# Kernel optimization log

Hardware: AMD Instinct MI355X
Metric: run time of the kernel (lower is better)

Reference implementation:

```python
import jax, jax.numpy as jnp
import numpy as np

EPS = 1e-12  # matches tf.math.l2_normalize epsilon

def _l2n(x, axis=-1):
    return x * jax.lax.rsqrt(jnp.maximum(jnp.sum(x * x, axis=axis, keepdims=True), EPS))


def setup_inputs() -> dict:
    key = jax.random.key(0)
    ks = jax.random.split(key, 8)
    B, T, D, N, M = 16, 1024, 1024, 2048, 256
    s = 1.0 / np.sqrt(D)
    return {
        "memory": jax.random.normal(ks[0], (N, M), jnp.float32),
        "controller_output": jax.random.normal(ks[1], (B, T, D), jnp.float32),
        "Wk": jax.random.normal(ks[2], (D, M), jnp.float32) * s,
        "bk": jnp.zeros((M,), jnp.float32),
        "We": jax.random.normal(ks[3], (D, M), jnp.float32) * s,
        "be": jnp.zeros((M,), jnp.float32),
        "Wa": jax.random.normal(ks[4], (D, M), jnp.float32) * s,
        "ba": jnp.zeros((M,), jnp.float32),
    }


def reference(memory, controller_output, Wk, bk, We, be, Wa, ba):
    B, T, _ = controller_output.shape
    # key: softmax over memory_size dim  -> [B,T,M]
    key = jax.nn.softmax(controller_output @ Wk + bk, axis=-1)
    # tf.keras.losses.cosine_similarity returns NEGATIVE cosine similarity
    kn = _l2n(key)          # [B,T,M]
    mn = _l2n(memory)       # [N,M]
    sims = -jnp.einsum('btm,nm->btn', kn, mn)          # [B,T,N]
    w = jax.nn.softmax(sims, axis=-1)                  # [B,T,N]
    erase = jax.nn.sigmoid(controller_output @ We + be)  # [B,T,M]
    add = jax.nn.relu(controller_output @ Wa + ba)       # [B,T,M]
    # mean over (B,T) of (1 - w*erase)*memory + w*add, without tiling memory:
    inv_bt = 1.0 / (B * T)
    we = jnp.einsum('btn,btm->nm', w, erase) * inv_bt   # mean of w \otimes erase
    wa = jnp.einsum('btn,btm->nm', w, add) * inv_bt     # mean of w \otimes add
    return memory * (1.0 - we) + wa                      # [N,M]
```

## Files before the change

### kernel.cpp

```cpp
#include <hip/hip_runtime.h>

#define DEV __device__ __forceinline__

using f32x4    = __attribute__((ext_vector_type(4))) float;
using bf16x8   = __attribute__((ext_vector_type(8))) short;
using float4_t = __attribute__((ext_vector_type(4))) float;
using ushort4_t = __attribute__((ext_vector_type(4))) unsigned short;
using ushort8_t = __attribute__((ext_vector_type(8))) unsigned short;

DEV unsigned short f2bf(float f) {
    unsigned int u = __builtin_bit_cast(unsigned int, f);
    u = (u + 0x7fffu + ((u >> 16) & 1u)) >> 16;
    return (unsigned short)u;
}
DEV float bf2f(unsigned short h) {
    unsigned int u = ((unsigned int)h) << 16;
    return __builtin_bit_cast(float, u);
}

DEV void gload_lds16(const void* g, void* l) {
    __builtin_amdgcn_global_load_lds((const __attribute__((address_space(1))) void*)g,
                                     (__attribute__((address_space(3))) void*)l, 16, 0, 0);
}

template<int TR, int TC, int NTH>
DEV void stage_tile(const unsigned short* __restrict__ src, long ld, long r0, long c0,
                    unsigned short* lds, int tid) {
    constexpr int LPR = (TC * 2) / 16;
    constexpr int RPI = 64 / LPR;
    constexpr int NISSUE = TR / RPI;
    constexpr int NW = NTH / 64;
    const int wid = tid >> 6, lane = tid & 63;
#pragma unroll
    for (int ii = 0; ii < NISSUE / NW; ++ii) {
        const int i = ii * NW + wid;
        const long row = r0 + (long)i * RPI + (lane / LPR);
        const unsigned short* g = src + row * ld + c0 + (lane % LPR) * 8;
        gload_lds16(g, lds + i * 512);
    }
}

__global__ void k0_cast_co(const float* __restrict__ in, unsigned short* __restrict__ out, long n4) {
    long i = (long)blockIdx.x * 256 + threadIdx.x;
    if (i >= n4) return;
    float4_t v = ((const float4_t*)in)[i];
    ushort4_t o;
#pragma unroll
    for (int j = 0; j < 4; ++j) o[j] = f2bf(v[j]);
    ((ushort4_t*)out)[i] = o;
}

__global__ void k0_prep_w(const float* __restrict__ Wk, const float* __restrict__ We,
                          const float* __restrict__ Wa, unsigned short* __restrict__ WcatT) {
    long idx = (long)blockIdx.x * 256 + threadIdx.x;
    int j = (int)(idx >> 10), d = (int)(idx & 1023);
    const float* W = (j < 256) ? Wk : (j < 512) ? We : Wa;
    int m = j & 255;
    WcatT[idx] = f2bf(W[(long)d * 256 + m]);
}

__global__ __launch_bounds__(256) void k0_mn(const float* __restrict__ memory,
                                             unsigned short* __restrict__ mn,
                                             float* __restrict__ S, int BT) {
    int gid = blockIdx.x * 256 + threadIdx.x;
    if (gid < BT) S[gid] = 0.f;
    int row = blockIdx.x * 4 + (threadIdx.x >> 6);
    int lane = threadIdx.x & 63;
    float4_t v = ((const float4_t*)(memory + (long)row * 256))[lane];
    float ss = v[0]*v[0] + v[1]*v[1] + v[2]*v[2] + v[3]*v[3];
#pragma unroll
    for (int d = 1; d < 64; d <<= 1) ss += __shfl_xor(ss, d);
    float sc = rsqrtf(fmaxf(ss, 1e-12f));
    ushort4_t o;
#pragma unroll
    for (int j = 0; j < 4; ++j) o[j] = f2bf(v[j] * sc);
    ((ushort4_t*)(mn + (long)row * 256))[lane] = o;
}

template<int BM, int BN, int BK>
__global__ __launch_bounds__(256, 3)
void k1_gemm_bias(const unsigned short* __restrict__ A, const unsigned short* __restrict__ BT,
                  float* __restrict__ C, int M, int N, int K,
                  const float* __restrict__ bk, const float* __restrict__ be,
                  const float* __restrict__ ba) {
    __shared__ __align__(16) unsigned short As[BM * BK];
    __shared__ __align__(16) unsigned short Bs[BN * BK];
    const int tid = threadIdx.x, lane = tid & 63, wid = tid >> 6;
    const long m0 = (long)blockIdx.x * BM, n0 = (long)blockIdx.y * BN;
    const int wr = (wid >> 1) * 64, wc = (wid & 1) * 64;
    f32x4 acc[4][4] = {};
    for (int kt = 0; kt < K; kt += BK) {
        stage_tile<BM, BK, 256>(A, K, m0, kt, As, tid);
        stage_tile<BN, BK, 256>(BT, K, n0, kt, Bs, tid);
        __syncthreads();
#pragma unroll
        for (int kk = 0; kk < BK; kk += 32) {
            const int klo = kk + (lane >> 4) * 8;
            bf16x8 af[4], bfr[4];
#pragma unroll
            for (int i = 0; i < 4; ++i) {
                af[i]  = *(const bf16x8*)&As[(wr + i * 16 + (lane & 15)) * BK + klo];
                bfr[i] = *(const bf16x8*)&Bs[(wc + i * 16 + (lane & 15)) * BK + klo];
            }
#pragma unroll
            for (int i = 0; i < 4; ++i)
#pragma unroll
                for (int j = 0; j < 4; ++j)
                    acc[i][j] = __builtin_amdgcn_mfma_f32_16x16x32_bf16(af[i], bfr[j], acc[i][j], 0, 0, 0);
        }
        __syncthreads();
    }
#pragma unroll
    for (int i = 0; i < 4; ++i) {
        const long rbase = m0 + wr + i * 16 + ((lane >> 4) * 4);
#pragma unroll
        for (int j = 0; j < 4; ++j) {
            const long col = n0 + wc + j * 16 + (lane & 15);
            float bias = (col < 256) ? bk[col] : (col < 512) ? be[col - 256] : ba[col - 512];
#pragma unroll
            for (int r = 0; r < 4; ++r)
                C[(rbase + r) * N + col] = acc[i][j][r] + bias;
        }
    }
}

__global__ __launch_bounds__(256) void k2_epilogue(const float* __restrict__ logits,
                                                   unsigned short* __restrict__ kn,
                                                   unsigned short* __restrict__ er,
                                                   unsigned short* __restrict__ ad) {
    const int row = blockIdx.x * 4 + (threadIdx.x >> 6);
    const int lane = threadIdx.x & 63;
    const float* L = logits + (long)row * 768;
    float4_t xk = ((const float4_t*)L)[lane];
    float4_t xe = ((const float4_t*)(L + 256))[lane];
    float4_t xa = ((const float4_t*)(L + 512))[lane];
    float mx = fmaxf(fmaxf(xk[0], xk[1]), fmaxf(xk[2], xk[3]));
#pragma unroll
    for (int d = 1; d < 64; d <<= 1) mx = fmaxf(mx, __shfl_xor(mx, d));
    float e[4]; float ss = 0.f;
#pragma unroll
    for (int j = 0; j < 4; ++j) { e[j] = __expf(xk[j] - mx); ss += e[j] * e[j]; }
#pragma unroll
    for (int d = 1; d < 64; d <<= 1) ss += __shfl_xor(ss, d);
    float sc = rsqrtf(ss);
    ushort4_t ok, oe, oa;
#pragma unroll
    for (int j = 0; j < 4; ++j) {
        ok[j] = f2bf(e[j] * sc);
        oe[j] = f2bf(1.f / (1.f + __expf(-xe[j])));
        oa[j] = f2bf(fmaxf(xa[j], 0.f));
    }
    ((ushort4_t*)(kn + (long)row * 256))[lane] = ok;
    ((ushort4_t*)(er + (long)row * 256))[lane] = oe;
    ((ushort4_t*)(ad + (long)row * 256))[lane] = oa;
}

template<int BM, int BN, int BK>
__global__ __launch_bounds__(256, 3)
void k3_gemm_sims(const unsigned short* __restrict__ A, const unsigned short* __restrict__ BT,
                  unsigned short* __restrict__ ET, float* __restrict__ S,
                  int M, int N, int K) {
    __shared__ __align__(16) unsigned short smem[BN * (BM + 8)];
    unsigned short* As = smem;
    unsigned short* Bs = smem + BM * BK;
    const int tid = threadIdx.x, lane = tid & 63, wid = tid >> 6;
    const long m0 = (long)blockIdx.x * BM, n0 = (long)blockIdx.y * BN;
    const int wr = (wid >> 1) * 64, wc = (wid & 1) * 64;
    f32x4 acc[4][4] = {};
    for (int kt = 0; kt < K; kt += BK) {
        stage_tile<BM, BK, 256>(A, K, m0, kt, As, tid);
        stage_tile<BN, BK, 256>(BT, K, n0, kt, Bs, tid);
        __syncthreads();
#pragma unroll
        for (int kk = 0; kk < BK; kk += 32) {
            const int klo = kk + (lane >> 4) * 8;
            bf16x8 af[4], bfr[4];
#pragma unroll
            for (int i = 0; i < 4; ++i) {
                af[i]  = *(const bf16x8*)&As[(wr + i * 16 + (lane & 15)) * BK + klo];
                bfr[i] = *(const bf16x8*)&Bs[(wc + i * 16 + (lane & 15)) * BK + klo];
            }
#pragma unroll
            for (int i = 0; i < 4; ++i)
#pragma unroll
                for (int j = 0; j < 4; ++j)
                    acc[i][j] = __builtin_amdgcn_mfma_f32_16x16x32_bf16(af[i], bfr[j], acc[i][j], 0, 0, 0);
        }
        __syncthreads();
    }
    float rs[4][4];
#pragma unroll
    for (int i = 0; i < 4; ++i)
#pragma unroll
        for (int r = 0; r < 4; ++r) rs[i][r] = 0.f;
    const int c16 = lane & 15, rq = (lane >> 4) * 4;
#pragma unroll
    for (int i = 0; i < 4; ++i) {
#pragma unroll
        for (int j = 0; j < 4; ++j) {
            ushort4_t pk;
#pragma unroll
            for (int r = 0; r < 4; ++r) {
                float e = __expf(-acc[i][j][r]);
                rs[i][r] += e;
                pk[r] = f2bf(e);
            }
            *(ushort4_t*)&smem[(wc + j * 16 + c16) * (BM + 8) + wr + i * 16 + rq] = pk;
        }
    }
#pragma unroll
    for (int d = 1; d < 16; d <<= 1)
#pragma unroll
        for (int i = 0; i < 4; ++i)
#pragma unroll
            for (int r = 0; r < 4; ++r) rs[i][r] += __shfl_xor(rs[i][r], d);
    if (c16 == 0) {
#pragma unroll
        for (int i = 0; i < 4; ++i)
#pragma unroll
            for (int r = 0; r < 4; ++r)
                atomicAdd(&S[m0 + wr + i * 16 + rq + r], rs[i][r]);
    }
    __syncthreads();
    constexpr int CPR = BM / 8;
#pragma unroll
    for (int it = 0; it < (BN * CPR) / 256; ++it) {
        int flat = it * 256 + tid;
        int c = flat / CPR, ch = flat % CPR;
        *(ushort8_t*)&ET[(n0 + c) * (long)M + m0 + ch * 8] =
            *(const ushort8_t*)&smem[c * (BM + 8) + ch * 8];
    }
}

__global__ __launch_bounds__(256) void k3c_scale_transpose(
        const unsigned short* __restrict__ er, const unsigned short* __restrict__ ad,
        const float* __restrict__ S, unsigned short* __restrict__ cat,
        float inv_bt, int BTr) {
    const unsigned short* src = blockIdx.y ? ad : er;
    unsigned short* dst = cat + (blockIdx.y ? (long)256 * BTr : 0);
    __shared__ __align__(16) unsigned short Tl[64][256 + 8];
    const int tid = threadIdx.x;
    const long kbase = (long)blockIdx.x * 64;
#pragma unroll
    for (int it = 0; it < 8; ++it) {
        int flat = it * 2048 + tid * 8;
        int kl = flat >> 8, m = flat & 255;
        float scale = inv_bt / S[kbase + kl];
        ushort8_t v = *(const ushort8_t*)&src[(kbase + kl) * 256 + m];
        ushort8_t o;
#pragma unroll
        for (int j = 0; j < 8; ++j) o[j] = f2bf(bf2f(v[j]) * scale);
        *(ushort8_t*)&Tl[kl][m] = o;
    }
    __syncthreads();
#pragma unroll
    for (int it = 0; it < 8; ++it) {
        int flat = it * 2048 + tid * 8;
        int m = flat >> 6, kc = flat & 63;
        ushort8_t o;
#pragma unroll
        for (int j = 0; j < 8; ++j) o[j] = Tl[kc + j][m];
        *(ushort8_t*)&dst[(long)m * BTr + kbase + kc] = o;
    }
}

template<int BM, int BN, int BK>
__global__ __launch_bounds__(512, 2)
void k4_gemm_cat(const unsigned short* __restrict__ A, const unsigned short* __restrict__ Bc,
                 float* __restrict__ pWE, float* __restrict__ pWA, long Ktot, int Kchunk) {
    __shared__ __align__(16) unsigned short As[BM * BK];
    __shared__ __align__(16) unsigned short Bs[BN * BK];
    const int tid = threadIdx.x, lane = tid & 63, wid = tid >> 6;
    const long n0 = (long)blockIdx.x * BM;
    const long mc0 = (long)blockIdx.y * BN;
    const int sk = blockIdx.z;
    const long kbeg = (long)sk * Kchunk;
    const int wr = (wid >> 2) * 64, wc = (wid & 3) * 32;
    f32x4 acc[4][2] = {};
    for (int kt = 0; kt < Kchunk; kt += BK) {
        stage_tile<BM, BK, 512>(A, Ktot, n0, kbeg + kt, As, tid);
        stage_tile<BN, BK, 512>(Bc, Ktot, mc0, kbeg + kt, Bs, tid);
        __syncthreads();
#pragma unroll
        for (int kk = 0; kk < BK; kk += 32) {
            const int klo = kk + (lane >> 4) * 8;
            bf16x8 af[4], bfr[2];
#pragma unroll
            for (int i = 0; i < 4; ++i)
                af[i] = *(const bf16x8*)&As[(wr + i * 16 + (lane & 15)) * BK + klo];
#pragma unroll
            for (int j = 0; j < 2; ++j)
                bfr[j] = *(const bf16x8*)&Bs[(wc + j * 16 + (lane & 15)) * BK + klo];
#pragma unroll
            for (int i = 0; i < 4; ++i)
#pragma unroll
                for (int j = 0; j < 2; ++j)
                    acc[i][j] = __builtin_amdgcn_mfma_f32_16x16x32_bf16(af[i], bfr[j], acc[i][j], 0, 0, 0);
        }
        __syncthreads();
    }
    float* dst = (blockIdx.y < 2) ? pWE : pWA;
    const long cb = (blockIdx.y & 1) * BN;
#pragma unroll
    for (int i = 0; i < 4; ++i) {
        const long row = n0 + wr + i * 16 + ((lane >> 4) * 4);
#pragma unroll
        for (int j = 0; j < 2; ++j) {
            const long col = cb + wc + j * 16 + (lane & 15);
#pragma unroll
            for (int r = 0; r < 4; ++r)
                dst[((long)sk * 2048 + row + r) * 256 + col] = acc[i][j][r];
        }
    }
}

__global__ void k5_finalize(const float* __restrict__ mem, const float* __restrict__ pWE,
                            const float* __restrict__ pWA, float* __restrict__ out,
                            int total, int splits) {
    int i = blockIdx.x * 256 + threadIdx.x;
    if (i * 4 >= total) return;
    float4_t we = {0.f, 0.f, 0.f, 0.f}, wa = {0.f, 0.f, 0.f, 0.f};
    for (int s = 0; s < splits; ++s) {
        we += ((const float4_t*)pWE)[(long)s * (total / 4) + i];
        wa += ((const float4_t*)pWA)[(long)s * (total / 4) + i];
    }
    float4_t m = ((const float4_t*)mem)[i];
    float4_t o;
#pragma unroll
    for (int j = 0; j < 4; ++j) o[j] = m[j] * (1.f - we[j]) + wa[j];
    ((float4_t*)out)[i] = o;
}

extern "C" void kernel_launch(void* const* d_in, const int* in_sizes, int n_in,
                              void* d_out, int out_size, void* d_ws, size_t ws_size,
                              hipStream_t stream) {
    const float* memory = (const float*)d_in[0];
    const float* co     = (const float*)d_in[1];
    const float* Wk     = (const float*)d_in[2];
    const float* bk     = (const float*)d_in[3];
    const float* We     = (const float*)d_in[4];
    const float* be     = (const float*)d_in[5];
    const float* Wa     = (const float*)d_in[6];
    const float* ba     = (const float*)d_in[7];
    float* out = (float*)d_out;

    constexpr int BT = 16384, D = 1024, N = 2048, Mm = 256, NC = 768;
    constexpr int SPLITK = 8;

    char* ws = (char*)d_ws;
    unsigned short* co_bf  = (unsigned short*)(ws + 0);
    float*          logits = (float*)(ws + 33554432);
    unsigned short* ET     = (unsigned short*)(ws + 0);
    float*          pWA    = (float*)(ws + 67108864);
    unsigned short* kn     = (unsigned short*)(ws + 83886080);
    float*          pWE    = (float*)(ws + 83886080);
    unsigned short* er     = (unsigned short*)(ws + 92274688);
    unsigned short* ad     = (unsigned short*)(ws + 100663296);
    unsigned short* mn     = (unsigned short*)(ws + 109051904);
    unsigned short* WcatT  = (unsigned short*)(ws + 110100480);
    float*          Sbuf   = (float*)(ws + 111673344);
    unsigned short* cat    = (unsigned short*)(ws + 111738880);

    k0_cast_co<<<(BT * (long)D / 4) / 256, 256, 0, stream>>>(co, co_bf, BT * (long)D / 4);
    k0_prep_w<<<(NC * D) / 256, 256, 0, stream>>>(Wk, We, Wa, WcatT);
    k0_mn<<<N / 4, 256, 0, stream>>>(memory, mn, Sbuf, BT);

    k1_gemm_bias<128, 128, 64><<<dim3(BT / 128, NC / 128), 256, 0, stream>>>(
        co_bf, WcatT, logits, BT, NC, D, bk, be, ba);

    k2_epilogue<<<BT / 4, 256, 0, stream>>>(logits, kn, er, ad);

    k3_gemm_sims<128, 128, 64><<<dim3(BT / 128, N / 128), 256, 0, stream>>>(
        kn, mn, ET, Sbuf, BT, N, Mm);

    k3c_scale_transpose<<<dim3(BT / 64, 2), 256, 0, stream>>>(
        er, ad, Sbuf, cat, 1.f / (float)BT, BT);

    k4_gemm_cat<128, 128, 64><<<dim3(N / 128, 512 / 128, SPLITK), 512, 0, stream>>>(
        ET, cat, pWE, pWA, (long)BT, BT / SPLITK);

    k5_finalize<<<(N * Mm / 4) / 256, 256, 0, stream>>>(memory, pWE, pWA, out, N * Mm, SPLITK);
}
```

Baseline: 275.9 us.

## Fuse projection GEMM with softmax/activation epilogue, swizzle LDS, retile split-K reduction

```diff
diff --git a/kernel.cpp b/kernel.cpp
--- a/kernel.cpp
+++ b/kernel.cpp
@@ -31,11 +31,13 @@
     constexpr int NISSUE = TR / RPI;
     constexpr int NW = NTH / 64;
     const int wid = tid >> 6, lane = tid & 63;
+    const int lr = lane / LPR;
+    const int lc = (lane % LPR) ^ lr;
 #pragma unroll
     for (int ii = 0; ii < NISSUE / NW; ++ii) {
         const int i = ii * NW + wid;
-        const long row = r0 + (long)i * RPI + (lane / LPR);
-        const unsigned short* g = src + row * ld + c0 + (lane % LPR) * 8;
+        const long row = r0 + (long)i * RPI + lr;
+        const unsigned short* g = src + row * ld + c0 + lc * 8;
         gload_lds16(g, lds + i * 512);
     }
 }
@@ -78,20 +80,23 @@
 }
 
 template<int BM, int BN, int BK>
-__global__ __launch_bounds__(256, 3)
-void k1_gemm_bias(const unsigned short* __restrict__ A, const unsigned short* __restrict__ BT,
-                  float* __restrict__ C, int M, int N, int K,
-                  const float* __restrict__ bk, const float* __restrict__ be,
-                  const float* __restrict__ ba) {
+__global__ __launch_bounds__(512, 4)
+void k1_fused(const unsigned short* __restrict__ A, const unsigned short* __restrict__ BT,
+              const float* __restrict__ bk, const float* __restrict__ be,
+              const float* __restrict__ ba, unsigned short* __restrict__ kn,
+              unsigned short* __restrict__ er, unsigned short* __restrict__ ad, int K) {
     __shared__ __align__(16) unsigned short As[BM * BK];
     __shared__ __align__(16) unsigned short Bs[BN * BK];
     const int tid = threadIdx.x, lane = tid & 63, wid = tid >> 6;
-    const long m0 = (long)blockIdx.x * BM, n0 = (long)blockIdx.y * BN;
-    const int wr = (wid >> 1) * 64, wc = (wid & 1) * 64;
+    const long m0 = (long)blockIdx.x * BM;
+    const int y = blockIdx.y;
+    const int wrg = wid >> 2, wcg = wid & 3;
+    const int wr = wrg * 64, wc = wcg * 64;
+    const int c16 = lane & 15, rq = (lane >> 4) * 4, swz = (lane & 7) * 8;
     f32x4 acc[4][4] = {};
     for (int kt = 0; kt < K; kt += BK) {
-        stage_tile<BM, BK, 256>(A, K, m0, kt, As, tid);
-        stage_tile<BN, BK, 256>(BT, K, n0, kt, Bs, tid);
+        stage_tile<BM, BK, 512>(A, K, m0, kt, As, tid);
+        stage_tile<BN, BK, 512>(BT, K, (long)y * BN, kt, Bs, tid);
         __syncthreads();
 #pragma unroll
         for (int kk = 0; kk < BK; kk += 32) {
@@ -99,8 +104,8 @@
             bf16x8 af[4], bfr[4];
 #pragma unroll
             for (int i = 0; i < 4; ++i) {
-                af[i]  = *(const bf16x8*)&As[(wr + i * 16 + (lane & 15)) * BK + klo];
-                bfr[i] = *(const bf16x8*)&Bs[(wc + i * 16 + (lane & 15)) * BK + klo];
+                af[i]  = *(const bf16x8*)&As[((wr + i * 16 + c16) * BK + klo) ^ swz];
+                bfr[i] = *(const bf16x8*)&Bs[((wc + i * 16 + c16) * BK + klo) ^ swz];
             }
 #pragma unroll
             for (int i = 0; i < 4; ++i)
@@ -110,53 +115,67 @@
         }
         __syncthreads();
     }
-#pragma unroll
-    for (int i = 0; i < 4; ++i) {
-        const long rbase = m0 + wr + i * 16 + ((lane >> 4) * 4);
-#pragma unroll
-        for (int j = 0; j < 4; ++j) {
-            const long col = n0 + wc + j * 16 + (lane & 15);
-            float bias = (col < 256) ? bk[col] : (col < 512) ? be[col - 256] : ba[col - 512];
-#pragma unroll
-            for (int r = 0; r < 4; ++r)
-                C[(rbase + r) * N + col] = acc[i][j][r] + bias;
-        }
-    }
-}
-
-__global__ __launch_bounds__(256) void k2_epilogue(const float* __restrict__ logits,
-                                                   unsigned short* __restrict__ kn,
-                                                   unsigned short* __restrict__ er,
-                                                   unsigned short* __restrict__ ad) {
-    const int row = blockIdx.x * 4 + (threadIdx.x >> 6);
-    const int lane = threadIdx.x & 63;
-    const float* L = logits + (long)row * 768;
-    float4_t xk = ((const float4_t*)L)[lane];
-    float4_t xe = ((const float4_t*)(L + 256))[lane];
-    float4_t xa = ((const float4_t*)(L + 512))[lane];
-    float mx = fmaxf(fmaxf(xk[0], xk[1]), fmaxf(xk[2], xk[3]));
-#pragma unroll
-    for (int d = 1; d < 64; d <<= 1) mx = fmaxf(mx, __shfl_xor(mx, d));
-    float e[4]; float ss = 0.f;
-#pragma unroll
-    for (int j = 0; j < 4; ++j) { e[j] = __expf(xk[j] - mx); ss += e[j] * e[j]; }
-#pragma unroll
-    for (int d = 1; d < 64; d <<= 1) ss += __shfl_xor(ss, d);
-    float sc = rsqrtf(ss);
-    ushort4_t ok, oe, oa;
-#pragma unroll
-    for (int j = 0; j < 4; ++j) {
-        ok[j] = f2bf(e[j] * sc);
-        oe[j] = f2bf(1.f / (1.f + __expf(-xe[j])));
-        oa[j] = f2bf(fmaxf(xa[j], 0.f));
-    }
-    ((ushort4_t*)(kn + (long)row * 256))[lane] = ok;
-    ((ushort4_t*)(er + (long)row * 256))[lane] = oe;
-    ((ushort4_t*)(ad + (long)row * 256))[lane] = oa;
+    const float* bias = (y == 0) ? bk : (y == 1) ? be : ba;
+    float bj[4];
+#pragma unroll
+    for (int j = 0; j < 4; ++j) bj[j] = bias[wc + j * 16 + c16];
+
+    if (y == 0) {
+        float* redsm = (float*)As;
+#pragma unroll
+        for (int i = 0; i < 4; ++i) {
+            float p[4] = {0.f, 0.f, 0.f, 0.f};
+#pragma unroll
+            for (int j = 0; j < 4; ++j)
+#pragma unroll
+                for (int r = 0; r < 4; ++r) {
+                    float e = __expf(acc[i][j][r] + bj[j]);
+                    acc[i][j][r] = e;
+                    p[r] += e * e;
+                }
+#pragma unroll
+            for (int d = 1; d < 16; d <<= 1)
+#pragma unroll
+                for (int r = 0; r < 4; ++r) p[r] += __shfl_xor(p[r], d);
+            if (c16 == 0) {
+#pragma unroll
+                for (int r = 0; r < 4; ++r)
+                    redsm[(wrg * 4 + wcg) * 64 + i * 16 + rq + r] = p[r];
+            }
+        }
+        __syncthreads();
+#pragma unroll
+        for (int i = 0; i < 4; ++i)
+#pragma unroll
+            for (int r = 0; r < 4; ++r) {
+                const int row64 = i * 16 + rq + r;
+                float tot = redsm[(wrg * 4 + 0) * 64 + row64] + redsm[(wrg * 4 + 1) * 64 + row64]
+                          + redsm[(wrg * 4 + 2) * 64 + row64] + redsm[(wrg * 4 + 3) * 64 + row64];
+                float sc = rsqrtf(tot);
+                const long row = m0 + wr + row64;
+#pragma unroll
+                for (int j = 0; j < 4; ++j)
+                    kn[row * 256 + wc + j * 16 + c16] = f2bf(acc[i][j][r] * sc);
+            }
+    } else {
+        unsigned short* dst = (y == 1) ? er : ad;
+#pragma unroll
+        for (int i = 0; i < 4; ++i)
+#pragma unroll
+            for (int r = 0; r < 4; ++r) {
+                const long row = m0 + wr + i * 16 + rq + r;
+#pragma unroll
+                for (int j = 0; j < 4; ++j) {
+                    float v = acc[i][j][r] + bj[j];
+                    float o = (y == 1) ? 1.f / (1.f + __expf(-v)) : fmaxf(v, 0.f);
+                    dst[row * 256 + wc + j * 16 + c16] = f2bf(o);
+                }
+            }
+    }
 }
 
 template<int BM, int BN, int BK>
-__global__ __launch_bounds__(256, 3)
+__global__ __launch_bounds__(256, 4)
 void k3_gemm_sims(const unsigned short* __restrict__ A, const unsigned short* __restrict__ BT,
                   unsigned short* __restrict__ ET, float* __restrict__ S,
                   int M, int N, int K) {
@@ -166,6 +185,7 @@
     const int tid = threadIdx.x, lane = tid & 63, wid = tid >> 6;
     const long m0 = (long)blockIdx.x * BM, n0 = (long)blockIdx.y * BN;
     const int wr = (wid >> 1) * 64, wc = (wid & 1) * 64;
+    const int c16 = lane & 15, rq = (lane >> 4) * 4, swz = (lane & 7) * 8;
     f32x4 acc[4][4] = {};
     for (int kt = 0; kt < K; kt += BK) {
         stage_tile<BM, BK, 256>(A, K, m0, kt, As, tid);
@@ -177,8 +197,8 @@
             bf16x8 af[4], bfr[4];
 #pragma unroll
             for (int i = 0; i < 4; ++i) {
-                af[i]  = *(const bf16x8*)&As[(wr + i * 16 + (lane & 15)) * BK + klo];
-                bfr[i] = *(const bf16x8*)&Bs[(wc + i * 16 + (lane & 15)) * BK + klo];
+                af[i]  = *(const bf16x8*)&As[((wr + i * 16 + c16) * BK + klo) ^ swz];
+                bfr[i] = *(const bf16x8*)&Bs[((wc + i * 16 + c16) * BK + klo) ^ swz];
             }
 #pragma unroll
             for (int i = 0; i < 4; ++i)
@@ -193,7 +213,6 @@
     for (int i = 0; i < 4; ++i)
 #pragma unroll
         for (int r = 0; r < 4; ++r) rs[i][r] = 0.f;
-    const int c16 = lane & 15, rq = (lane >> 4) * 4;
 #pragma unroll
     for (int i = 0; i < 4; ++i) {
 #pragma unroll
@@ -265,9 +284,9 @@
 }
 
 template<int BM, int BN, int BK>
-__global__ __launch_bounds__(512, 2)
+__global__ __launch_bounds__(512, 4)
 void k4_gemm_cat(const unsigned short* __restrict__ A, const unsigned short* __restrict__ Bc,
-                 float* __restrict__ pWE, float* __restrict__ pWA, long Ktot, int Kchunk) {
+                 unsigned short* __restrict__ pP, long Ktot, int Kchunk) {
     __shared__ __align__(16) unsigned short As[BM * BK];
     __shared__ __align__(16) unsigned short Bs[BN * BK];
     const int tid = threadIdx.x, lane = tid & 63, wid = tid >> 6;
@@ -275,8 +294,9 @@
     const long mc0 = (long)blockIdx.y * BN;
     const int sk = blockIdx.z;
     const long kbeg = (long)sk * Kchunk;
-    const int wr = (wid >> 2) * 64, wc = (wid & 3) * 32;
-    f32x4 acc[4][2] = {};
+    const int wr = (wid >> 1) * 64, wc = (wid & 1) * 64;
+    const int c16 = lane & 15, rq = (lane >> 4) * 4, swz = (lane & 7) * 8;
+    f32x4 acc[4][4] = {};
     for (int kt = 0; kt < Kchunk; kt += BK) {
         stage_tile<BM, BK, 512>(A, Ktot, n0, kbeg + kt, As, tid);
         stage_tile<BN, BK, 512>(Bc, Ktot, mc0, kbeg + kt, Bs, tid);
@@ -284,51 +304,51 @@
 #pragma unroll
         for (int kk = 0; kk < BK; kk += 32) {
             const int klo = kk + (lane >> 4) * 8;
-            bf16x8 af[4], bfr[2];
+            bf16x8 af[4], bfr[4];
+#pragma unroll
+            for (int i = 0; i < 4; ++i) {
+                af[i]  = *(const bf16x8*)&As[((wr + i * 16 + c16) * BK + klo) ^ swz];
+                bfr[i] = *(const bf16x8*)&Bs[((wc + i * 16 + c16) * BK + klo) ^ swz];
+            }
 #pragma unroll
             for (int i = 0; i < 4; ++i)
-                af[i] = *(const bf16x8*)&As[(wr + i * 16 + (lane & 15)) * BK + klo];
-#pragma unroll
-            for (int j = 0; j < 2; ++j)
-                bfr[j] = *(const bf16x8*)&Bs[(wc + j * 16 + (lane & 15)) * BK + klo];
-#pragma unroll
-            for (int i = 0; i < 4; ++i)
-#pragma unroll
-                for (int j = 0; j < 2; ++j)
+#pragma unroll
+                for (int j = 0; j < 4; ++j)
                     acc[i][j] = __builtin_amdgcn_mfma_f32_16x16x32_bf16(af[i], bfr[j], acc[i][j], 0, 0, 0);
         }
         __syncthreads();
     }
-    float* dst = (blockIdx.y < 2) ? pWE : pWA;
-    const long cb = (blockIdx.y & 1) * BN;
 #pragma unroll
     for (int i = 0; i < 4; ++i) {
-        const long row = n0 + wr + i * 16 + ((lane >> 4) * 4);
-#pragma unroll
-        for (int j = 0; j < 2; ++j) {
-            const long col = cb + wc + j * 16 + (lane & 15);
+        const long row = n0 + wr + i * 16 + rq;
+#pragma unroll
+        for (int j = 0; j < 4; ++j) {
+            const long col = mc0 + wc + j * 16 + c16;
 #pragma unroll
             for (int r = 0; r < 4; ++r)
-                dst[((long)sk * 2048 + row + r) * 256 + col] = acc[i][j][r];
-        }
-    }
-}
-
-__global__ void k5_finalize(const float* __restrict__ mem, const float* __restrict__ pWE,
-                            const float* __restrict__ pWA, float* __restrict__ out,
-                            int total, int splits) {
-    int i = blockIdx.x * 256 + threadIdx.x;
-    if (i * 4 >= total) return;
-    float4_t we = {0.f, 0.f, 0.f, 0.f}, wa = {0.f, 0.f, 0.f, 0.f};
+                pP[((long)sk * 2048 + row + r) * 512 + col] = f2bf(acc[i][j][r]);
+        }
+    }
+}
+
+__global__ __launch_bounds__(256) void k5_finalize(const float* __restrict__ mem,
+                                                   const unsigned short* __restrict__ pP,
+                                                   float* __restrict__ out, int splits) {
+    int idx = blockIdx.x * 256 + threadIdx.x;
+    int n = idx >> 6, m4 = (idx & 63) * 4;
+    float we[4] = {0.f, 0.f, 0.f, 0.f}, wa[4] = {0.f, 0.f, 0.f, 0.f};
     for (int s = 0; s < splits; ++s) {
-        we += ((const float4_t*)pWE)[(long)s * (total / 4) + i];
-        wa += ((const float4_t*)pWA)[(long)s * (total / 4) + i];
-    }
-    float4_t m = ((const float4_t*)mem)[i];
+        const unsigned short* row = pP + ((long)s * 2048 + n) * 512;
+        ushort4_t ve = *(const ushort4_t*)&row[m4];
+        ushort4_t va = *(const ushort4_t*)&row[256 + m4];
+#pragma unroll
+        for (int j = 0; j < 4; ++j) { we[j] += bf2f(ve[j]); wa[j] += bf2f(va[j]); }
+    }
+    float4_t mv = ((const float4_t*)mem)[idx];
     float4_t o;
 #pragma unroll
-    for (int j = 0; j < 4; ++j) o[j] = m[j] * (1.f - we[j]) + wa[j];
-    ((float4_t*)out)[i] = o;
+    for (int j = 0; j < 4; ++j) o[j] = mv[j] * (1.f - we[j]) + wa[j];
+    ((float4_t*)out)[idx] = o;
 }
 
 extern "C" void kernel_launch(void* const* d_in, const int* in_sizes, int n_in,
@@ -344,40 +364,36 @@
     const float* ba     = (const float*)d_in[7];
     float* out = (float*)d_out;
 
-    constexpr int BT = 16384, D = 1024, N = 2048, Mm = 256, NC = 768;
-    constexpr int SPLITK = 8;
+    constexpr int BT = 16384, D = 1024, N = 2048, NC = 768;
+    constexpr int SPLITK = 16;
 
     char* ws = (char*)d_ws;
     unsigned short* co_bf  = (unsigned short*)(ws + 0);
-    float*          logits = (float*)(ws + 33554432);
     unsigned short* ET     = (unsigned short*)(ws + 0);
-    float*          pWA    = (float*)(ws + 67108864);
-    unsigned short* kn     = (unsigned short*)(ws + 83886080);
-    float*          pWE    = (float*)(ws + 83886080);
-    unsigned short* er     = (unsigned short*)(ws + 92274688);
-    unsigned short* ad     = (unsigned short*)(ws + 100663296);
-    unsigned short* mn     = (unsigned short*)(ws + 109051904);
-    unsigned short* WcatT  = (unsigned short*)(ws + 110100480);
-    float*          Sbuf   = (float*)(ws + 111673344);
-    unsigned short* cat    = (unsigned short*)(ws + 111738880);
+    unsigned short* kn     = (unsigned short*)(ws + 67108864);
+    unsigned short* er     = (unsigned short*)(ws + 75497472);
+    unsigned short* ad     = (unsigned short*)(ws + 83886080);
+    unsigned short* mn     = (unsigned short*)(ws + 92274688);
+    unsigned short* WcatT  = (unsigned short*)(ws + 93323264);
+    float*          Sbuf   = (float*)(ws + 94896128);
+    unsigned short* cat    = (unsigned short*)(ws + 94961664);
+    unsigned short* pP     = (unsigned short*)(ws + 111738880);
 
     k0_cast_co<<<(BT * (long)D / 4) / 256, 256, 0, stream>>>(co, co_bf, BT * (long)D / 4);
     k0_prep_w<<<(NC * D) / 256, 256, 0, stream>>>(Wk, We, Wa, WcatT);
     k0_mn<<<N / 4, 256, 0, stream>>>(memory, mn, Sbuf, BT);
 
-    k1_gemm_bias<128, 128, 64><<<dim3(BT / 128, NC / 128), 256, 0, stream>>>(
-        co_bf, WcatT, logits, BT, NC, D, bk, be, ba);
-
-    k2_epilogue<<<BT / 4, 256, 0, stream>>>(logits, kn, er, ad);
+    k1_fused<128, 256, 64><<<dim3(BT / 128, 3), 512, 0, stream>>>(
+        co_bf, WcatT, bk, be, ba, kn, er, ad, D);
 
     k3_gemm_sims<128, 128, 64><<<dim3(BT / 128, N / 128), 256, 0, stream>>>(
-        kn, mn, ET, Sbuf, BT, N, Mm);
+        kn, mn, ET, Sbuf, BT, N, 256);
 
     k3c_scale_transpose<<<dim3(BT / 64, 2), 256, 0, stream>>>(
         er, ad, Sbuf, cat, 1.f / (float)BT, BT);
 
-    k4_gemm_cat<128, 128, 64><<<dim3(N / 128, 512 / 128, SPLITK), 512, 0, stream>>>(
-        ET, cat, pWE, pWA, (long)BT, BT / SPLITK);
-
-    k5_finalize<<<(N * Mm / 4) / 256, 256, 0, stream>>>(memory, pWE, pWA, out, N * Mm, SPLITK);
-}
+    k4_gemm_cat<256, 128, 64><<<dim3(N / 256, 512 / 128, SPLITK), 512, 0, stream>>>(
+        ET, cat, pP, (long)BT, BT / SPLITK);
+
+    k5_finalize<<<(N * 256 / 4) / 256, 256, 0, stream>>>(memory, pP, out, SPLITK);
+}
```

Measured after the change: 239.8 us. -13.1%, faster.
